# Performance work log

Measured on AMD Instinct MI355X. Metric: run time of the kernel, lower is better.

## Reference

```python
import jax, jax.numpy as jnp
import numpy as np
from jax import lax

B, C, T = 256, 4, 4096
PATCH = 16
H = 64          # hidden_dim == motif_dim
K = 128         # codebook_size
NC = 2          # num_classes
TAU_MAX = 1.0
SR = 256.0


def setup_inputs() -> dict:
    key = jax.random.key(0)
    ks = jax.random.split(key, 16)
    s = 0.05
    return {
        "x": jax.random.normal(ks[0], (B, C, T), jnp.float32),
        "codebook": jax.random.normal(ks[1], (K, H), jnp.float32) * 0.5,
        "W_enc": jax.random.normal(ks[2], (PATCH, H), jnp.float32) * s,
        "b_enc": jnp.zeros((H,), jnp.float32),
        "W_enc2": jax.random.normal(ks[3], (H, H), jnp.float32) * s,
        "b_enc2": jnp.zeros((H,), jnp.float32),
        "W_lat": jax.random.normal(ks[4], (H, H), jnp.float32) * s,
        "b_lat": jnp.zeros((H,), jnp.float32),
        "W_time": jax.random.normal(ks[5], (H, H), jnp.float32) * s,
        "b_time": jnp.zeros((H,), jnp.float32),
        "W_e1": jax.random.normal(ks[6], (2 * H, H), jnp.float32) * s,
        "b_e1": jnp.zeros((H,), jnp.float32),
        "W_e2": jax.random.normal(ks[7], (H, 2), jnp.float32) * s,
        "b_e2": jnp.zeros((2,), jnp.float32),
        "W_adj": jax.random.normal(ks[8], (H, H), jnp.float32) * s,
        "W_self": jax.random.normal(ks[9], (H, H), jnp.float32) * s,
        "b_ode": jnp.zeros((H,), jnp.float32),
        "ln_g": jnp.ones((H,), jnp.float32),
        "ln_b": jnp.zeros((H,), jnp.float32),
        "W_h1": jax.random.normal(ks[10], (H, H), jnp.float32) * s,
        "b_h1": jnp.zeros((H,), jnp.float32),
        "W_h2": jax.random.normal(ks[11], (H, NC), jnp.float32) * s,
        "b_h2": jnp.zeros((NC,), jnp.float32),
    }


def reference(x, codebook, W_enc, b_enc, W_enc2, b_enc2, W_lat, b_lat,
              W_time, b_time, W_e1, b_e1, W_e2, b_e2,
              W_adj, W_self, b_ode, ln_g, ln_b, W_h1, b_h1, W_h2, b_h2):
    sg = lax.stop_gradient
    b, c, t = x.shape
    p = t // PATCH  # patches after /16 downsampling

    # --- motif VAE encoder (patchify conv, stride == kernel == 16) ---
    flat = x.reshape(b * c, p, PATCH)                       # [N,P,16]
    z_e = jax.nn.gelu(flat @ W_enc + b_enc) @ W_enc2 + b_enc2  # [N,P,H]

    # --- vector quantization ---
    d = ((z_e ** 2).sum(-1, keepdims=True)
         - 2.0 * (z_e @ codebook.T)
         + (codebook ** 2).sum(-1))                        # [N,P,K]
    idx = jnp.argmin(d, axis=-1)                            # [N,P]
    z_q = codebook[idx]                                     # [N,P,H]
    commit_loss = jnp.mean((z_e - sg(z_q)) ** 2)
    codebook_loss = jnp.mean((sg(z_e) - z_q) ** 2)
    z_q_st = z_e + sg(z_q - z_e)                            # straight-through

    # --- latent projection + Fourier time embedding ---
    h = (z_q_st @ W_lat + b_lat).reshape(b, c, p, H)        # [B,C,P,H]
    patch_time = jnp.linspace(0.0, t / SR, p).astype(h.dtype)
    half = H // 2
    freqs = jnp.exp(jnp.linspace(0.0, np.log(1000.0), half)).astype(h.dtype)
    ang = patch_time[:, None] * freqs[None, :]              # [P,H/2]
    temb = jnp.concatenate([jnp.sin(ang), jnp.cos(ang)], -1) @ W_time + b_time
    h = h + temb[None, None]                                # broadcast [B,C,P,H]

    # --- lagged edge scorer over channels ---
    feat = h.mean(axis=2)                                   # [B,C,H]
    pair = jnp.concatenate([
        jnp.broadcast_to(feat[:, :, None, :], (b, c, c, H)),
        jnp.broadcast_to(feat[:, None, :, :], (b, c, c, H)),
    ], axis=-1)                                             # [B,C,C,2H]
    e = jax.nn.gelu(pair @ W_e1 + b_e1) @ W_e2 + b_e2       # [B,C,C,2]
    edge_probs = jax.nn.sigmoid(e[..., 0])
    tau = TAU_MAX * jax.nn.sigmoid(e[..., 1])
    adjacency = edge_probs * (1.0 - jnp.eye(c, dtype=h.dtype))
    focal_scores = -tau.sum(axis=-1)                        # [B,C]

    # --- adjacency-conditioned graph ODE, RK4 over t_grid ---
    h0 = h[:, :, 0, :]                                      # [B,C,H]

    def f(s):
        return jnp.tanh(jnp.einsum('bij,bjh->bih', adjacency, s @ W_adj)
                        + s @ W_self + b_ode)

    def step(s, dt):
        k1 = f(s)
        k2 = f(s + 0.5 * dt * k1)
        k3 = f(s + 0.5 * dt * k2)
        k4 = f(s + dt * k3)
        s2 = s + (dt / 6.0) * (k1 + 2.0 * k2 + 2.0 * k3 + k4)
        return s2, s2

    dts = jnp.diff(patch_time)
    _, traj = lax.scan(step, h0, dts)                       # [P-1,B,C,H]
    trajectory = jnp.concatenate([h0[None], traj], axis=0)  # [P,B,C,H]

    # pooled = trajectory.mean over (time, channel)
    pooled = trajectory.mean(axis=(0, 2))                   # [B,H]

    # --- head: LayerNorm -> Linear -> GELU -> Linear ---
    mu = pooled.mean(-1, keepdims=True)
    var = ((pooled - mu) ** 2).mean(-1, keepdims=True)
    normed = (pooled - mu) * lax.rsqrt(var + 1e-5) * ln_g + ln_b
    logits = jax.nn.gelu(normed @ W_h1 + b_h1) @ W_h2 + b_h2  # [B,NC]

    return logits, focal_scores, tau, commit_loss, codebook_loss
```

## Files before the change

kernel.cpp:

```cpp
#include <hip/hip_runtime.h>

#define NB 256
#define NC_ 4
#define NT 4096
#define NPATCH 16
#define NP 256
#define NH 64
#define NK 128

typedef float f32x2 __attribute__((ext_vector_type(2)));
typedef float f32x4 __attribute__((ext_vector_type(4)));

#define OFF_TEMBM  0
#define OFF_TEMB0  64
#define OFF_MT     128
#define OFF_CC     8320
#define OFF_ZQSUM  8448
#define OFF_ZQ0    73984
#define OFF_COMMIT 139520
#define OFF_ADJ    140544
#define OFF_H0     144640

__device__ __forceinline__ float tanh_fast(float x) {
    float e = __expf(2.0f * x);
    return 1.0f - __fdividef(2.0f, e + 1.0f);
}
__device__ __forceinline__ float gelu_f(float x) {
    float x3 = x * x * x;
    float t = tanh_fast(0.7978845608028654f * (x + 0.044715f * x3));
    return 0.5f * x * (1.0f + t);
}
__device__ __forceinline__ float sigmoid_f(float x) {
    return __fdividef(1.0f, 1.0f + __expf(-x));
}

__global__ void k0_prep(const float* __restrict__ cb, const float* __restrict__ W_enc2,
                        const float* __restrict__ b_enc2, const float* __restrict__ W_time,
                        const float* __restrict__ b_time, float* __restrict__ ws) {
    const int t = threadIdx.x;
    if (blockIdx.x == 0) {
        __shared__ float ps[8][32], pc[8][32], sm[32], cm[32];
        const int k = t & 31, pg = t >> 5;
        const float step = 16.0f / 255.0f;
        const float lstep = (float)6.907755278982137 / 31.0f;
        const float fr = expf((float)k * lstep);
        float s_acc = 0.f, c_acc = 0.f;
        for (int pp = 0; pp < 32; ++pp) {
            int p = (pg << 5) + pp;
            float ang = ((float)p * step) * fr;
            s_acc += sinf(ang);
            c_acc += cosf(ang);
        }
        ps[pg][k] = s_acc; pc[pg][k] = c_acc;
        __syncthreads();
        if (t < 32) {
            float s = 0.f, c2 = 0.f;
            for (int g = 0; g < 8; ++g) { s += ps[g][t]; c2 += pc[g][t]; }
            sm[t] = s * (1.0f / 256.0f);
            cm[t] = c2 * (1.0f / 256.0f);
        }
        __syncthreads();
        if (t < 64) {
            float tm = b_time[t];
            float t0 = b_time[t];
            for (int kk = 0; kk < 32; ++kk) {
                tm = fmaf(sm[kk], W_time[kk * 64 + t], tm);
                tm = fmaf(cm[kk], W_time[(32 + kk) * 64 + t], tm);
                t0 += W_time[(32 + kk) * 64 + t];
            }
            ws[OFF_TEMBM + t] = tm;
            ws[OFF_TEMB0 + t] = t0;
        }
        if (t >= 128) {
            int j = t - 128;
            float cbn = 0.f, bc2 = 0.f;
            for (int hh = 0; hh < 64; ++hh) {
                float cv = cb[j * 64 + hh];
                cbn = fmaf(cv, cv, cbn);
                bc2 = fmaf(b_enc2[hh], cv, bc2);
            }
            ws[OFF_CC + j] = cbn - 2.0f * bc2;
        }
    } else {
        int oid = (blockIdx.x - 1) * 256 + t;
        int j = oid >> 6, kk = oid & 63;
        float acc = 0.f;
        for (int hh = 0; hh < 64; ++hh)
            acc = fmaf(W_enc2[kk * 64 + hh], cb[j * 64 + hh], acc);
        ws[OFF_MT + oid] = acc;
    }
}

__global__ __launch_bounds__(256) void k1_encvq(
    const float* __restrict__ x, const float* __restrict__ cb,
    const float* __restrict__ W_enc, const float* __restrict__ b_enc,
    const float* __restrict__ W_enc2, const float* __restrict__ b_enc2,
    float* __restrict__ ws) {
    __shared__ float sWeT[1024];
    __shared__ float sW2[4096];
    __shared__ float sMT[8192];
    __shared__ float sCC[128];
    __shared__ float sB1[64];
    __shared__ float sB2[64];
    __shared__ int   sCnt[128];
    __shared__ float sScr[4];
    __shared__ int   sIdx0;

    const int t = threadIdx.x;
    const int bc = blockIdx.x;

    for (int i = t; i < 1024; i += 256) {
        int hh = i >> 4, kk = i & 15;
        sWeT[i] = W_enc[kk * 64 + hh];
    }
    for (int i = t; i < 4096; i += 256) sW2[i] = W_enc2[i];
    for (int i = t; i < 8192; i += 256) sMT[i] = ws[OFF_MT + i];
    if (t < 128) { sCC[t] = ws[OFF_CC + t]; sCnt[t] = 0; }
    if (t < 64) sB1[t] = b_enc[t];
    else if (t < 128) sB2[t - 64] = b_enc2[t - 64];
    __syncthreads();

    const float4* xp = (const float4*)(x + (size_t)bc * NT + t * NPATCH);
    float4 xa = xp[0], xb = xp[1], xc = xp[2], xd = xp[3];
    float xx[16] = {xa.x,xa.y,xa.z,xa.w, xb.x,xb.y,xb.z,xb.w,
                    xc.x,xc.y,xc.z,xc.w, xd.x,xd.y,xd.z,xd.w};

    float e1[64];
    #pragma unroll
    for (int hh = 0; hh < 64; ++hh) {
        const float4* w4 = (const float4*)(&sWeT[hh * 16]);
        float4 wa = w4[0], wb = w4[1], wc = w4[2], wd = w4[3];
        float a = sB1[hh];
        a = fmaf(xx[0],  wa.x, a); a = fmaf(xx[1],  wa.y, a);
        a = fmaf(xx[2],  wa.z, a); a = fmaf(xx[3],  wa.w, a);
        a = fmaf(xx[4],  wb.x, a); a = fmaf(xx[5],  wb.y, a);
        a = fmaf(xx[6],  wb.z, a); a = fmaf(xx[7],  wb.w, a);
        a = fmaf(xx[8],  wc.x, a); a = fmaf(xx[9],  wc.y, a);
        a = fmaf(xx[10], wc.z, a); a = fmaf(xx[11], wc.w, a);
        a = fmaf(xx[12], wd.x, a); a = fmaf(xx[13], wd.y, a);
        a = fmaf(xx[14], wd.z, a); a = fmaf(xx[15], wd.w, a);
        e1[hh] = gelu_f(a);
    }

    float ze2 = 0.f;
    #pragma unroll 1
    for (int ch = 0; ch < 4; ++ch) {
        const int hb = ch << 4;
        float z[16];
        #pragma unroll
        for (int i = 0; i < 16; ++i) z[i] = sB2[hb + i];
        #pragma unroll
        for (int kk = 0; kk < 64; ++kk) {
            float ek = e1[kk];
            const float4* w4 = (const float4*)(&sW2[kk * 64 + hb]);
            float4 wa = w4[0], wb = w4[1], wc = w4[2], wd = w4[3];
            z[0]  = fmaf(ek, wa.x, z[0]);  z[1]  = fmaf(ek, wa.y, z[1]);
            z[2]  = fmaf(ek, wa.z, z[2]);  z[3]  = fmaf(ek, wa.w, z[3]);
            z[4]  = fmaf(ek, wb.x, z[4]);  z[5]  = fmaf(ek, wb.y, z[5]);
            z[6]  = fmaf(ek, wb.z, z[6]);  z[7]  = fmaf(ek, wb.w, z[7]);
            z[8]  = fmaf(ek, wc.x, z[8]);  z[9]  = fmaf(ek, wc.y, z[9]);
            z[10] = fmaf(ek, wc.z, z[10]); z[11] = fmaf(ek, wc.w, z[11]);
            z[12] = fmaf(ek, wd.x, z[12]); z[13] = fmaf(ek, wd.y, z[13]);
            z[14] = fmaf(ek, wd.z, z[14]); z[15] = fmaf(ek, wd.w, z[15]);
        }
        #pragma unroll
        for (int i = 0; i < 16; ++i) ze2 = fmaf(z[i], z[i], ze2);
    }

    float bestscore = 3.4e38f; int best = 0;
    #pragma unroll 2
    for (int j = 0; j < 128; ++j) {
        const float4* m4 = (const float4*)(&sMT[j * 64]);
        float d0 = 0.f, d1 = 0.f, d2 = 0.f, d3 = 0.f;
        #pragma unroll
        for (int kk = 0; kk < 16; ++kk) {
            float4 m = m4[kk];
            d0 = fmaf(e1[4 * kk],     m.x, d0);
            d1 = fmaf(e1[4 * kk + 1], m.y, d1);
            d2 = fmaf(e1[4 * kk + 2], m.z, d2);
            d3 = fmaf(e1[4 * kk + 3], m.w, d3);
        }
        float score = fmaf(-2.0f, (d0 + d1) + (d2 + d3), sCC[j]);
        if (score < bestscore) { bestscore = score; best = j; }
    }

    float cp = ze2 + bestscore;
    #pragma unroll
    for (int off = 32; off; off >>= 1) cp += __shfl_xor(cp, off);
    if ((t & 63) == 0) sScr[t >> 6] = cp;
    atomicAdd(&sCnt[best], 1);
    if (t == 0) sIdx0 = best;
    __syncthreads();

    if (t < 64) {
        float acc = 0.f;
        for (int j = 0; j < 128; ++j)
            acc = fmaf((float)sCnt[j], cb[j * 64 + t], acc);
        ws[OFF_ZQSUM + bc * 64 + t] = acc;
    } else if (t < 128) {
        int hh = t - 64;
        ws[OFF_ZQ0 + bc * 64 + hh] = cb[sIdx0 * 64 + hh];
    } else if (t == 128) {
        ws[OFF_COMMIT + bc] = (sScr[0] + sScr[1]) + (sScr[2] + sScr[3]);
    }
}

__global__ __launch_bounds__(256) void k2_graph(
    const float* __restrict__ W_lat, const float* __restrict__ b_lat,
    const float* __restrict__ W_e1, const float* __restrict__ b_e1,
    const float* __restrict__ W_e2, const float* __restrict__ b_e2,
    float* __restrict__ ws, float* __restrict__ out) {
    __shared__ float sWlat[4096];
    __shared__ float sWe1[8192];
    __shared__ float sWe2[128];
    __shared__ float sfeat[256];
    __shared__ float shid[1024];
    __shared__ float stau[16];
    __shared__ float scr2[4];

    const int t = threadIdx.x, b = blockIdx.x;
    const int c = t >> 6, h = t & 63;
    for (int i = t; i < 4096; i += 256) sWlat[i] = W_lat[i];
    for (int i = t; i < 8192; i += 256) sWe1[i] = W_e1[i];
    if (t < 128) sWe2[t] = W_e2[t];
    __syncthreads();

    const int bc = b * 4 + c;
    float zqm = ws[OFF_ZQSUM + bc * 64 + h] * (1.0f / 256.0f);
    float zq0 = ws[OFF_ZQ0 + bc * 64 + h];
    float base = b_lat[h];
    float ft = base + ws[OFF_TEMBM + h];
    float h0 = base + ws[OFF_TEMB0 + h];
    #pragma unroll
    for (int kk = 0; kk < 64; ++kk) {
        float w = sWlat[kk * 64 + h];
        ft = fmaf(__shfl(zqm, kk), w, ft);
        h0 = fmaf(__shfl(zq0, kk), w, h0);
    }
    ws[OFF_H0 + bc * 64 + h] = h0;
    sfeat[c * 64 + h] = ft;
    __syncthreads();

    #pragma unroll
    for (int pp = 0; pp < 4; ++pp) {
        const int p = pp * 4 + c;
        const int i = p >> 2, j = p & 3;
        float hv = b_e1[h];
        #pragma unroll
        for (int kk = 0; kk < 64; ++kk) {
            hv = fmaf(sfeat[i * 64 + kk], sWe1[kk * 64 + h], hv);
            hv = fmaf(sfeat[j * 64 + kk], sWe1[(64 + kk) * 64 + h], hv);
        }
        shid[p * 64 + h] = gelu_f(hv);
    }
    __syncthreads();

    if (t < 16) {
        const int p = t, i = p >> 2, j = p & 3;
        float e0 = 0.f, ev = 0.f;
        #pragma unroll
        for (int hh = 0; hh < 64; ++hh) {
            float g = shid[p * 64 + hh];
            e0 = fmaf(g, sWe2[hh * 2], e0);
            ev = fmaf(g, sWe2[hh * 2 + 1], ev);
        }
        e0 += b_e2[0]; ev += b_e2[1];
        float tv = sigmoid_f(ev);
        out[1536 + b * 16 + p] = tv;
        stau[p] = tv;
        ws[OFF_ADJ + b * 16 + p] = (i == j) ? 0.f : sigmoid_f(e0);
    }
    __syncthreads();
    if (t < 4) {
        out[512 + b * 4 + t] =
            -(((stau[t * 4] + stau[t * 4 + 1]) + stau[t * 4 + 2]) + stau[t * 4 + 3]);
    }
    if (b == 0) {
        float cp = (ws[OFF_COMMIT + t] + ws[OFF_COMMIT + 256 + t]) +
                   (ws[OFF_COMMIT + 512 + t] + ws[OFF_COMMIT + 768 + t]);
        #pragma unroll
        for (int off = 32; off; off >>= 1) cp += __shfl_xor(cp, off);
        if ((t & 63) == 0) scr2[t >> 6] = cp;
        __syncthreads();
        if (t == 0) {
            float m = ((scr2[0] + scr2[1]) + (scr2[2] + scr2[3])) * (1.0f / 16777216.0f);
            out[5632] = m; out[5633] = m;
        }
    }
}

__global__ __launch_bounds__(512, 2) void k3_ode(
    const float* __restrict__ W_adj, const float* __restrict__ W_self, const float* __restrict__ b_ode,
    const float* __restrict__ ln_g, const float* __restrict__ ln_b,
    const float* __restrict__ W_h1, const float* __restrict__ b_h1,
    const float* __restrict__ W_h2, const float* __restrict__ b_h2,
    const float* __restrict__ ws, float* __restrict__ out) {
    __shared__ float sS[256];
    __shared__ float sPU[2][4][64][2];
    __shared__ float sPV[2][4][64][2];

    const int t = threadIdx.x, b = blockIdx.x;
    const int w = t >> 6;
    const int q = w & 3;
    const int j = w >> 2;
    const int h = t & 63;

    f32x2 Wa2[16], Wsf2[16];
    #pragma unroll
    for (int i = 0; i < 16; ++i) {
        const int k0 = (j << 5) + (i << 1);
        Wa2[i]  = f32x2{W_adj[k0 * 64 + h],  W_adj[(k0 + 1) * 64 + h]};
        Wsf2[i] = f32x2{W_self[k0 * 64 + h], W_self[(k0 + 1) * 64 + h]};
    }

    const float* adjp = ws + OFF_ADJ + b * 16;
    const int c1 = (q + 1) & 3, c2 = (q + 2) & 3, c3 = (q + 3) & 3;
    const float A1 = adjp[q * 4 + c1];
    const float A2 = adjp[q * 4 + c2];
    const float A3 = adjp[q * 4 + c3];
    const float bo = b_ode[h];

    float s = ws[OFF_H0 + (b * 4 + q) * 64 + h];
    float pool = s;
    const bool own = ((h >> 5) == j);
    if (own) sS[(q << 6) + h] = s;

    const float step = 16.0f / 255.0f;
    const int kb0 = (q << 6) + (j << 5);

    auto feval = [&](int par) __attribute__((always_inline)) -> float {
        f32x2 uA = {0.f, 0.f}, uB = {0.f, 0.f};
        f32x2 vA = {0.f, 0.f}, vB = {0.f, 0.f};
        #pragma unroll
        for (int i = 0; i < 8; ++i) {
            f32x4 sc = *(const f32x4*)&sS[kb0 + (i << 2)];
            f32x2 lo = __builtin_shufflevector(sc, sc, 0, 1);
            f32x2 hi = __builtin_shufflevector(sc, sc, 2, 3);
            uA = __builtin_elementwise_fma(lo, Wa2[2 * i],      uA);
            uB = __builtin_elementwise_fma(hi, Wa2[2 * i + 1],  uB);
            vA = __builtin_elementwise_fma(lo, Wsf2[2 * i],     vA);
            vB = __builtin_elementwise_fma(hi, Wsf2[2 * i + 1], vB);
        }
        f32x2 uT = uA + uB, vT = vA + vB;
        sPU[par][q][h][j] = uT.x + uT.y;
        sPV[par][q][h][j] = vT.x + vT.y;
        __syncthreads();
        f32x2 p1 = *(const f32x2*)&sPU[par][c1][h][0];
        f32x2 p2 = *(const f32x2*)&sPU[par][c2][h][0];
        f32x2 p3 = *(const f32x2*)&sPU[par][c3][h][0];
        f32x2 pv = *(const f32x2*)&sPV[par][q][h][0];
        float m = pv.x + pv.y;
        m = fmaf(A1, p1.x + p1.y, m);
        m = fmaf(A2, p2.x + p2.y, m);
        m = fmaf(A3, p3.x + p3.y, m);
        return tanh_fast(m + bo);
    };

    #pragma unroll 1
    for (int it = 0; it < 255; ++it) {
        float dt = (float)(it + 1) * step - (float)it * step;
        float hdt = 0.5f * dt;
        float r1 = feval(0);
        if (own) sS[(q << 6) + h] = fmaf(hdt, r1, s);
        float r2 = feval(1);
        if (own) sS[(q << 6) + h] = fmaf(hdt, r2, s);
        float r3 = feval(0);
        if (own) sS[(q << 6) + h] = fmaf(dt, r3, s);
        float r4 = feval(1);
        s = fmaf(dt * (1.0f / 6.0f), ((r1 + r4) + 2.0f * (r2 + r3)), s);
        pool += s;
        if (own) sS[(q << 6) + h] = s;
    }

    __syncthreads();
    if (j == 0) sS[(q << 6) + h] = pool;
    __syncthreads();

    if (w == 0) {
        float pd = ((sS[h] + sS[64 + h]) + (sS[128 + h] + sS[192 + h])) * (1.0f / 1024.0f);
        float mu = pd;
        #pragma unroll
        for (int off = 32; off; off >>= 1) mu += __shfl_xor(mu, off);
        mu *= (1.0f / 64.0f);
        float dv = pd - mu;
        float vr = dv * dv;
        #pragma unroll
        for (int off = 32; off; off >>= 1) vr += __shfl_xor(vr, off);
        vr *= (1.0f / 64.0f);
        float nr = dv * rsqrtf(vr + 1e-5f) * ln_g[h] + ln_b[h];
        sS[h] = nr;
        float acc = b_h1[h];
        #pragma unroll
        for (int i = 0; i < 16; ++i) {
            f32x4 nv = *(const f32x4*)&sS[i << 2];
            acc = fmaf(nv.x, W_h1[(4 * i + 0) * 64 + h], acc);
            acc = fmaf(nv.y, W_h1[(4 * i + 1) * 64 + h], acc);
            acc = fmaf(nv.z, W_h1[(4 * i + 2) * 64 + h], acc);
            acc = fmaf(nv.w, W_h1[(4 * i + 3) * 64 + h], acc);
        }
        float g1 = gelu_f(acc);
        float l0 = g1 * W_h2[h * 2];
        float l1 = g1 * W_h2[h * 2 + 1];
        #pragma unroll
        for (int off = 32; off; off >>= 1) { l0 += __shfl_xor(l0, off); l1 += __shfl_xor(l1, off); }
        if (h == 0) {
            out[b * 2]     = l0 + b_h2[0];
            out[b * 2 + 1] = l1 + b_h2[1];
        }
    }
}

extern "C" void kernel_launch(void* const* d_in, const int* in_sizes, int n_in,
                              void* d_out, int out_size, void* d_ws, size_t ws_size,
                              hipStream_t stream) {
    (void)in_sizes; (void)n_in; (void)out_size; (void)ws_size;
    const float* x      = (const float*)d_in[0];
    const float* cb     = (const float*)d_in[1];
    const float* W_enc  = (const float*)d_in[2];
    const float* b_enc  = (const float*)d_in[3];
    const float* W_enc2 = (const float*)d_in[4];
    const float* b_enc2 = (const float*)d_in[5];
    const float* W_lat  = (const float*)d_in[6];
    const float* b_lat  = (const float*)d_in[7];
    const float* W_time = (const float*)d_in[8];
    const float* b_time = (const float*)d_in[9];
    const float* W_e1   = (const float*)d_in[10];
    const float* b_e1   = (const float*)d_in[11];
    const float* W_e2   = (const float*)d_in[12];
    const float* b_e2   = (const float*)d_in[13];
    const float* W_adj  = (const float*)d_in[14];
    const float* W_self = (const float*)d_in[15];
    const float* b_ode  = (const float*)d_in[16];
    const float* ln_g   = (const float*)d_in[17];
    const float* ln_b   = (const float*)d_in[18];
    const float* W_h1   = (const float*)d_in[19];
    const float* b_h1   = (const float*)d_in[20];
    const float* W_h2   = (const float*)d_in[21];
    const float* b_h2   = (const float*)d_in[22];
    float* out = (float*)d_out;
    float* ws  = (float*)d_ws;

    hipLaunchKernelGGL(k0_prep, dim3(33), dim3(256), 0, stream,
                       cb, W_enc2, b_enc2, W_time, b_time, ws);
    hipLaunchKernelGGL(k1_encvq, dim3(1024), dim3(256), 0, stream,
                       x, cb, W_enc, b_enc, W_enc2, b_enc2, ws);
    hipLaunchKernelGGL(k2_graph, dim3(256), dim3(256), 0, stream,
                       W_lat, b_lat, W_e1, b_e1, W_e2, b_e2, ws, out);
    hipLaunchKernelGGL(k3_ode, dim3(256), dim3(512), 0, stream,
                       W_adj, W_self, b_ode, ln_g, ln_b, W_h1, b_h1, W_h2, b_h2, ws, out);
}
```

Before: 572.0 us.

## Process two patches per thread in encoder/VQ kernel using packed f32x2 FMAs

The encoder+VQ kernel now runs 128 threads per block, and each thread handles two patches packed into f32x2 vectors. This lets the compiler emit packed FP32 FMAs and amortizes each shared-memory weight load over two patches. It also reshapes the ODE feval sum into a tree to shorten the dependency chain. The cost is doubled per-thread register pressure (e12 is 128 floats), which with launch bounds of (128,2) may cause spills or lower occupancy.

```diff
diff --git a/kernel.cpp b/kernel.cpp
--- a/kernel.cpp
+++ b/kernel.cpp
@@ -91,7 +91,7 @@
     }
 }
 
-__global__ __launch_bounds__(256) void k1_encvq(
+__global__ __launch_bounds__(128, 2) void k1_encvq(
     const float* __restrict__ x, const float* __restrict__ cb,
     const float* __restrict__ W_enc, const float* __restrict__ b_enc,
     const float* __restrict__ W_enc2, const float* __restrict__ b_enc2,
@@ -103,93 +103,119 @@
     __shared__ float sB1[64];
     __shared__ float sB2[64];
     __shared__ int   sCnt[128];
-    __shared__ float sScr[4];
+    __shared__ float sScr[2];
     __shared__ int   sIdx0;
 
     const int t = threadIdx.x;
     const int bc = blockIdx.x;
 
-    for (int i = t; i < 1024; i += 256) {
+    for (int i = t; i < 1024; i += 128) {
         int hh = i >> 4, kk = i & 15;
         sWeT[i] = W_enc[kk * 64 + hh];
     }
-    for (int i = t; i < 4096; i += 256) sW2[i] = W_enc2[i];
-    for (int i = t; i < 8192; i += 256) sMT[i] = ws[OFF_MT + i];
+    for (int i = t; i < 4096; i += 128) sW2[i] = W_enc2[i];
+    for (int i = t; i < 8192; i += 128) sMT[i] = ws[OFF_MT + i];
     if (t < 128) { sCC[t] = ws[OFF_CC + t]; sCnt[t] = 0; }
     if (t < 64) sB1[t] = b_enc[t];
-    else if (t < 128) sB2[t - 64] = b_enc2[t - 64];
-    __syncthreads();
-
-    const float4* xp = (const float4*)(x + (size_t)bc * NT + t * NPATCH);
-    float4 xa = xp[0], xb = xp[1], xc = xp[2], xd = xp[3];
-    float xx[16] = {xa.x,xa.y,xa.z,xa.w, xb.x,xb.y,xb.z,xb.w,
-                    xc.x,xc.y,xc.z,xc.w, xd.x,xd.y,xd.z,xd.w};
-
-    float e1[64];
+    else sB2[t - 64] = b_enc2[t - 64];
+    __syncthreads();
+
+    const float4* xp0 = (const float4*)(x + (size_t)bc * NT + t * NPATCH);
+    const float4* xp1 = (const float4*)(x + (size_t)bc * NT + (t + 128) * NPATCH);
+    float4 a0 = xp0[0], a1 = xp0[1], a2 = xp0[2], a3 = xp0[3];
+    float4 b0 = xp1[0], b1v = xp1[1], b2 = xp1[2], b3 = xp1[3];
+    f32x2 xp2[16] = {
+        {a0.x,b0.x},{a0.y,b0.y},{a0.z,b0.z},{a0.w,b0.w},
+        {a1.x,b1v.x},{a1.y,b1v.y},{a1.z,b1v.z},{a1.w,b1v.w},
+        {a2.x,b2.x},{a2.y,b2.y},{a2.z,b2.z},{a2.w,b2.w},
+        {a3.x,b3.x},{a3.y,b3.y},{a3.z,b3.z},{a3.w,b3.w}};
+
+    f32x2 e12[64];
     #pragma unroll
     for (int hh = 0; hh < 64; ++hh) {
         const float4* w4 = (const float4*)(&sWeT[hh * 16]);
         float4 wa = w4[0], wb = w4[1], wc = w4[2], wd = w4[3];
-        float a = sB1[hh];
-        a = fmaf(xx[0],  wa.x, a); a = fmaf(xx[1],  wa.y, a);
-        a = fmaf(xx[2],  wa.z, a); a = fmaf(xx[3],  wa.w, a);
-        a = fmaf(xx[4],  wb.x, a); a = fmaf(xx[5],  wb.y, a);
-        a = fmaf(xx[6],  wb.z, a); a = fmaf(xx[7],  wb.w, a);
-        a = fmaf(xx[8],  wc.x, a); a = fmaf(xx[9],  wc.y, a);
-        a = fmaf(xx[10], wc.z, a); a = fmaf(xx[11], wc.w, a);
-        a = fmaf(xx[12], wd.x, a); a = fmaf(xx[13], wd.y, a);
-        a = fmaf(xx[14], wd.z, a); a = fmaf(xx[15], wd.w, a);
-        e1[hh] = gelu_f(a);
-    }
-
-    float ze2 = 0.f;
+        f32x2 acc = {sB1[hh], sB1[hh]};
+        acc = __builtin_elementwise_fma(xp2[0],  f32x2{wa.x, wa.x}, acc);
+        acc = __builtin_elementwise_fma(xp2[1],  f32x2{wa.y, wa.y}, acc);
+        acc = __builtin_elementwise_fma(xp2[2],  f32x2{wa.z, wa.z}, acc);
+        acc = __builtin_elementwise_fma(xp2[3],  f32x2{wa.w, wa.w}, acc);
+        acc = __builtin_elementwise_fma(xp2[4],  f32x2{wb.x, wb.x}, acc);
+        acc = __builtin_elementwise_fma(xp2[5],  f32x2{wb.y, wb.y}, acc);
+        acc = __builtin_elementwise_fma(xp2[6],  f32x2{wb.z, wb.z}, acc);
+        acc = __builtin_elementwise_fma(xp2[7],  f32x2{wb.w, wb.w}, acc);
+        acc = __builtin_elementwise_fma(xp2[8],  f32x2{wc.x, wc.x}, acc);
+        acc = __builtin_elementwise_fma(xp2[9],  f32x2{wc.y, wc.y}, acc);
+        acc = __builtin_elementwise_fma(xp2[10], f32x2{wc.z, wc.z}, acc);
+        acc = __builtin_elementwise_fma(xp2[11], f32x2{wc.w, wc.w}, acc);
+        acc = __builtin_elementwise_fma(xp2[12], f32x2{wd.x, wd.x}, acc);
+        acc = __builtin_elementwise_fma(xp2[13], f32x2{wd.y, wd.y}, acc);
+        acc = __builtin_elementwise_fma(xp2[14], f32x2{wd.z, wd.z}, acc);
+        acc = __builtin_elementwise_fma(xp2[15], f32x2{wd.w, wd.w}, acc);
+        e12[hh] = f32x2{gelu_f(acc.x), gelu_f(acc.y)};
+    }
+
+    f32x2 ze2 = {0.f, 0.f};
     #pragma unroll 1
     for (int ch = 0; ch < 4; ++ch) {
         const int hb = ch << 4;
-        float z[16];
-        #pragma unroll
-        for (int i = 0; i < 16; ++i) z[i] = sB2[hb + i];
+        f32x2 z2[16];
+        #pragma unroll
+        for (int i = 0; i < 16; ++i) { float bz = sB2[hb + i]; z2[i] = f32x2{bz, bz}; }
         #pragma unroll
         for (int kk = 0; kk < 64; ++kk) {
-            float ek = e1[kk];
+            f32x2 ek = e12[kk];
             const float4* w4 = (const float4*)(&sW2[kk * 64 + hb]);
             float4 wa = w4[0], wb = w4[1], wc = w4[2], wd = w4[3];
-            z[0]  = fmaf(ek, wa.x, z[0]);  z[1]  = fmaf(ek, wa.y, z[1]);
-            z[2]  = fmaf(ek, wa.z, z[2]);  z[3]  = fmaf(ek, wa.w, z[3]);
-            z[4]  = fmaf(ek, wb.x, z[4]);  z[5]  = fmaf(ek, wb.y, z[5]);
-            z[6]  = fmaf(ek, wb.z, z[6]);  z[7]  = fmaf(ek, wb.w, z[7]);
-            z[8]  = fmaf(ek, wc.x, z[8]);  z[9]  = fmaf(ek, wc.y, z[9]);
-            z[10] = fmaf(ek, wc.z, z[10]); z[11] = fmaf(ek, wc.w, z[11]);
-            z[12] = fmaf(ek, wd.x, z[12]); z[13] = fmaf(ek, wd.y, z[13]);
-            z[14] = fmaf(ek, wd.z, z[14]); z[15] = fmaf(ek, wd.w, z[15]);
-        }
-        #pragma unroll
-        for (int i = 0; i < 16; ++i) ze2 = fmaf(z[i], z[i], ze2);
-    }
-
-    float bestscore = 3.4e38f; int best = 0;
+            z2[0]  = __builtin_elementwise_fma(ek, f32x2{wa.x, wa.x}, z2[0]);
+            z2[1]  = __builtin_elementwise_fma(ek, f32x2{wa.y, wa.y}, z2[1]);
+            z2[2]  = __builtin_elementwise_fma(ek, f32x2{wa.z, wa.z}, z2[2]);
+            z2[3]  = __builtin_elementwise_fma(ek, f32x2{wa.w, wa.w}, z2[3]);
+            z2[4]  = __builtin_elementwise_fma(ek, f32x2{wb.x, wb.x}, z2[4]);
+            z2[5]  = __builtin_elementwise_fma(ek, f32x2{wb.y, wb.y}, z2[5]);
+            z2[6]  = __builtin_elementwise_fma(ek, f32x2{wb.z, wb.z}, z2[6]);
+            z2[7]  = __builtin_elementwise_fma(ek, f32x2{wb.w, wb.w}, z2[7]);
+            z2[8]  = __builtin_elementwise_fma(ek, f32x2{wc.x, wc.x}, z2[8]);
+            z2[9]  = __builtin_elementwise_fma(ek, f32x2{wc.y, wc.y}, z2[9]);
+            z2[10] = __builtin_elementwise_fma(ek, f32x2{wc.z, wc.z}, z2[10]);
+            z2[11] = __builtin_elementwise_fma(ek, f32x2{wc.w, wc.w}, z2[11]);
+            z2[12] = __builtin_elementwise_fma(ek, f32x2{wd.x, wd.x}, z2[12]);
+            z2[13] = __builtin_elementwise_fma(ek, f32x2{wd.y, wd.y}, z2[13]);
+            z2[14] = __builtin_elementwise_fma(ek, f32x2{wd.z, wd.z}, z2[14]);
+            z2[15] = __builtin_elementwise_fma(ek, f32x2{wd.w, wd.w}, z2[15]);
+        }
+        #pragma unroll
+        for (int i = 0; i < 16; ++i) ze2 = __builtin_elementwise_fma(z2[i], z2[i], ze2);
+    }
+
+    float best0 = 3.4e38f, best1 = 3.4e38f; int idx0 = 0, idx1 = 0;
     #pragma unroll 2
     for (int j = 0; j < 128; ++j) {
         const float4* m4 = (const float4*)(&sMT[j * 64]);
-        float d0 = 0.f, d1 = 0.f, d2 = 0.f, d3 = 0.f;
+        f32x2 dA = {0.f, 0.f}, dB = {0.f, 0.f}, dC = {0.f, 0.f}, dD = {0.f, 0.f};
         #pragma unroll
         for (int kk = 0; kk < 16; ++kk) {
             float4 m = m4[kk];
-            d0 = fmaf(e1[4 * kk],     m.x, d0);
-            d1 = fmaf(e1[4 * kk + 1], m.y, d1);
-            d2 = fmaf(e1[4 * kk + 2], m.z, d2);
-            d3 = fmaf(e1[4 * kk + 3], m.w, d3);
-        }
-        float score = fmaf(-2.0f, (d0 + d1) + (d2 + d3), sCC[j]);
-        if (score < bestscore) { bestscore = score; best = j; }
-    }
-
-    float cp = ze2 + bestscore;
+            dA = __builtin_elementwise_fma(e12[4 * kk],     f32x2{m.x, m.x}, dA);
+            dB = __builtin_elementwise_fma(e12[4 * kk + 1], f32x2{m.y, m.y}, dB);
+            dC = __builtin_elementwise_fma(e12[4 * kk + 2], f32x2{m.z, m.z}, dC);
+            dD = __builtin_elementwise_fma(e12[4 * kk + 3], f32x2{m.w, m.w}, dD);
+        }
+        f32x2 dT = (dA + dB) + (dC + dD);
+        float cc = sCC[j];
+        float s0 = fmaf(-2.0f, dT.x, cc);
+        float s1 = fmaf(-2.0f, dT.y, cc);
+        if (s0 < best0) { best0 = s0; idx0 = j; }
+        if (s1 < best1) { best1 = s1; idx1 = j; }
+    }
+
+    float cp = (ze2.x + best0) + (ze2.y + best1);
     #pragma unroll
     for (int off = 32; off; off >>= 1) cp += __shfl_xor(cp, off);
     if ((t & 63) == 0) sScr[t >> 6] = cp;
-    atomicAdd(&sCnt[best], 1);
-    if (t == 0) sIdx0 = best;
+    atomicAdd(&sCnt[idx0], 1);
+    atomicAdd(&sCnt[idx1], 1);
+    if (t == 0) sIdx0 = idx0;
     __syncthreads();
 
     if (t < 64) {
@@ -197,11 +223,10 @@
         for (int j = 0; j < 128; ++j)
             acc = fmaf((float)sCnt[j], cb[j * 64 + t], acc);
         ws[OFF_ZQSUM + bc * 64 + t] = acc;
-    } else if (t < 128) {
+        if (t == 0) ws[OFF_COMMIT + bc] = sScr[0] + sScr[1];
+    } else {
         int hh = t - 64;
         ws[OFF_ZQ0 + bc * 64 + hh] = cb[sIdx0 * 64 + hh];
-    } else if (t == 128) {
-        ws[OFF_COMMIT + bc] = (sScr[0] + sScr[1]) + (sScr[2] + sScr[3]);
     }
 }
 
@@ -349,11 +374,9 @@
         f32x2 p2 = *(const f32x2*)&sPU[par][c2][h][0];
         f32x2 p3 = *(const f32x2*)&sPU[par][c3][h][0];
         f32x2 pv = *(const f32x2*)&sPV[par][q][h][0];
-        float m = pv.x + pv.y;
-        m = fmaf(A1, p1.x + p1.y, m);
-        m = fmaf(A2, p2.x + p2.y, m);
-        m = fmaf(A3, p3.x + p3.y, m);
-        return tanh_fast(m + bo);
+        float m01 = (pv.x + pv.y) + A1 * (p1.x + p1.y);
+        float m23 = A2 * (p2.x + p2.y) + A3 * (p3.x + p3.y);
+        return tanh_fast((m01 + m23) + bo);
     };
 
     #pragma unroll 1
@@ -442,7 +465,7 @@
 
     hipLaunchKernelGGL(k0_prep, dim3(33), dim3(256), 0, stream,
                        cb, W_enc2, b_enc2, W_time, b_time, ws);
-    hipLaunchKernelGGL(k1_encvq, dim3(1024), dim3(256), 0, stream,
+    hipLaunchKernelGGL(k1_encvq, dim3(1024), dim3(128), 0, stream,
                        x, cb, W_enc, b_enc, W_enc2, b_enc2, ws);
     hipLaunchKernelGGL(k2_graph, dim3(256), dim3(256), 0, stream,
                        W_lat, b_lat, W_e1, b_e1, W_e2, b_e2, ws, out);
```

After: 642.7 us. 1.12x slower.
